# Performance work log

Hardware: AMD Instinct MI355X
Metric: run time of the kernel (lower is better)

The kernel has to match this reference:

```python
import jax, jax.numpy as jnp
import numpy as np

EPS = 1e-5
N_GRID = 519840
N_MESH = 5882
D_DATA = 256
D_NODE = 128
D_EDGE = 2
H = 128


def _ln(x, g, b):
    mu = jnp.mean(x, axis=-1, keepdims=True)
    v = jnp.var(x, axis=-1, keepdims=True)
    return (x - mu) * jax.lax.rsqrt(v + EPS) * g + b


def _ffn(x, Wr, br, W1, b1, W2, b2, g, bn):
    # FFN: norm(residual(x) + Linear(ReLU(Linear(x))))
    res = x if Wr is None else x @ Wr + br
    h = jax.nn.relu(x @ W1 + b1) @ W2 + b2
    return _ln(res + h, g, bn)


def setup_inputs() -> dict:
    key = jax.random.key(0)
    ks = jax.random.split(key, 32)
    s = 0.02

    def w(k, shape):
        return jax.random.normal(k, shape, dtype=jnp.float32) * s

    inp = {}
    inp["x"] = jax.random.normal(ks[0], (N_GRID, D_DATA), dtype=jnp.float32)
    inp["edge_attr"] = jax.random.normal(ks[1], (N_GRID, D_EDGE), dtype=jnp.float32)
    row = jnp.arange(N_GRID, dtype=jnp.int32)
    col = jax.random.randint(ks[2], (N_GRID,), N_GRID, N_GRID + N_MESH, dtype=jnp.int32)
    inp["edge_index"] = jnp.stack([row, col], 0)
    inp["num_mesh"] = N_MESH

    # node_encoder FFN: 256 -> 128 (residual Linear since in != out)
    inp["enc_Wr"] = w(ks[3], (D_DATA, D_NODE)); inp["enc_br"] = jnp.zeros((D_NODE,), jnp.float32)
    inp["enc_W1"] = w(ks[4], (D_DATA, H)); inp["enc_b1"] = jnp.zeros((H,), jnp.float32)
    inp["enc_W2"] = w(ks[5], (H, D_NODE)); inp["enc_b2"] = jnp.zeros((D_NODE,), jnp.float32)
    inp["enc_g"] = jnp.ones((D_NODE,), jnp.float32); inp["enc_bn"] = jnp.zeros((D_NODE,), jnp.float32)

    # edge model FFN: 2*128+2=258 -> 2
    de_in = 2 * D_NODE + D_EDGE
    inp["em_Wr"] = w(ks[6], (de_in, D_EDGE)); inp["em_br"] = jnp.zeros((D_EDGE,), jnp.float32)
    inp["em_W1"] = w(ks[7], (de_in, H)); inp["em_b1"] = jnp.zeros((H,), jnp.float32)
    inp["em_W2"] = w(ks[8], (H, D_EDGE)); inp["em_b2"] = jnp.zeros((D_EDGE,), jnp.float32)
    inp["em_g"] = jnp.ones((D_EDGE,), jnp.float32); inp["em_bn"] = jnp.zeros((D_EDGE,), jnp.float32)

    # node_mlp_1 FFN: 130 -> 130 (identity residual)
    d1 = D_NODE + D_EDGE
    inp["n1_W1"] = w(ks[9], (d1, H)); inp["n1_b1"] = jnp.zeros((H,), jnp.float32)
    inp["n1_W2"] = w(ks[10], (H, d1)); inp["n1_b2"] = jnp.zeros((d1,), jnp.float32)
    inp["n1_g"] = jnp.ones((d1,), jnp.float32); inp["n1_bn"] = jnp.zeros((d1,), jnp.float32)

    # node_mlp_2 FFN: 258 -> 128 (residual Linear)
    d2 = 2 * D_NODE + D_EDGE
    inp["n2_Wr"] = w(ks[11], (d2, D_NODE)); inp["n2_br"] = jnp.zeros((D_NODE,), jnp.float32)
    inp["n2_W1"] = w(ks[12], (d2, H)); inp["n2_b1"] = jnp.zeros((H,), jnp.float32)
    inp["n2_W2"] = w(ks[13], (H, D_NODE)); inp["n2_b2"] = jnp.zeros((D_NODE,), jnp.float32)
    inp["n2_g"] = jnp.ones((D_NODE,), jnp.float32); inp["n2_bn"] = jnp.zeros((D_NODE,), jnp.float32)
    return inp


def reference(x, edge_attr, edge_index, num_mesh,
              enc_Wr, enc_br, enc_W1, enc_b1, enc_W2, enc_b2, enc_g, enc_bn,
              em_Wr, em_br, em_W1, em_b1, em_W2, em_b2, em_g, em_bn,
              n1_W1, n1_b1, n1_W2, n1_b2, n1_g, n1_bn,
              n2_Wr, n2_br, n2_W1, n2_b1, n2_W2, n2_b2, n2_g, n2_bn):
    n_grid = x.shape[0]
    x_hat = _ffn(x, enc_Wr, enc_br, enc_W1, enc_b1, enc_W2, enc_b2, enc_g, enc_bn)
    nodes = jnp.concatenate([x_hat, jnp.zeros((num_mesh, x_hat.shape[1]), x_hat.dtype)], 0)

    row, col = edge_index[0], edge_index[1]
    src = nodes[row]   # [E, 128]
    dest = nodes[col]  # [E, 128]

    # EdgeModel: updated edge_attr
    e = _ffn(jnp.concatenate([src, dest, edge_attr], 1),
             em_Wr, em_br, em_W1, em_b1, em_W2, em_b2, em_g, em_bn) + edge_attr

    # NodeModel: per-edge message, scatter-mean to target nodes
    m = _ffn(jnp.concatenate([src, e], 1),
             None, None, n1_W1, n1_b1, n1_W2, n1_b2, n1_g, n1_bn)  # [E, 130]
    n_tot = n_grid + num_mesh
    s = jax.ops.segment_sum(m, col, num_segments=n_tot)
    cnt = jax.ops.segment_sum(jnp.ones((col.shape[0], 1), m.dtype), col, num_segments=n_tot)
    agg = s / jnp.maximum(cnt, 1.0)  # scatter-mean

    nodes2 = _ffn(jnp.concatenate([nodes, agg], 1),
                  n2_Wr, n2_br, n2_W1, n2_b1, n2_W2, n2_b2, n2_g, n2_bn) + nodes
    return nodes2[n_grid:]
```

## Files before the change

### kernel.cpp

```cpp
#include <hip/hip_runtime.h>
#include <hip/hip_bf16.h>

#define EDGES   519840
#define NGRID   519840
#define NMESH   5882

typedef short s8v __attribute__((ext_vector_type(8)));
typedef float f4v __attribute__((ext_vector_type(4)));

#define OFF_ENC1   0
#define OFF_ENCW2  65536
#define OFF_EM1    81920
#define OFF_N11    104960
#define OFF_N12    125440
#define PACK_EL    143872
#define GSUM_BYTE_OFF  (PACK_EL*2)
#define GSUM_BYTES     (NMESH*130*4)
#define CNT_BYTE_OFF   (GSUM_BYTE_OFF + GSUM_BYTES)
#define CNT_BYTES      (NMESH*4)

__device__ __forceinline__ float b2f(short s) {
  unsigned int u = ((unsigned int)(unsigned short)s) << 16;
  float f; __builtin_memcpy(&f, &u, 4); return f;
}
__device__ __forceinline__ short f2b(float f) {
  __hip_bfloat16 h = __float2bfloat16(f);
  short s; __builtin_memcpy(&s, &h, 2); return s;
}

struct PArgs {
  const float *enc_Wr, *enc_W1, *enc_W2;
  const float *em_Wr, *em_W1, *em_b1, *em_br;
  const float *n1_W1, *n1_b1, *n1_W2;
  short* dst;
};

__global__ __launch_bounds__(256) void kPack(PArgs p) {
  int g = blockIdx.x * 256 + threadIdx.x;
  if (g >= 17984) return;
  short* dst = p.dst;
  if (g < 8192) {
    int s = g >> 10; int rem = g & 1023; int t = rem >> 6; int l = rem & 63;
    int qq = l >> 4, n = (t << 4) + (l & 15);
    s8v v;
    #pragma unroll
    for (int j = 0; j < 8; ++j) {
      int k = s*32 + qq*8 + j;
      v[j] = (n < 128) ? f2b(p.enc_Wr[k*128 + n]) : f2b(p.enc_W1[k*128 + (n-128)]);
    }
    ((s8v*)(dst + OFF_ENC1))[g] = v;
  } else if (g < 10240) {
    int g2 = g - 8192;
    int s = g2 >> 9; int t = (g2 >> 6) & 7; int l = g2 & 63;
    int qq = l >> 4, n = (t << 4) + (l & 15);
    s8v v;
    #pragma unroll
    for (int j = 0; j < 8; ++j) { int k = s*32 + qq*8 + j; v[j] = f2b(p.enc_W2[k*128 + n]); }
    ((s8v*)(dst + OFF_ENCW2))[g2] = v;
  } else if (g < 13120) {
    int g3 = g - 10240;
    int s = g3 / 576; int rem = g3 - s*576; int t = rem >> 6; int l = rem & 63;
    int qq = l >> 4, n = (t << 4) + (l & 15);
    s8v v;
    #pragma unroll
    for (int j = 0; j < 8; ++j) {
      int k = s*32 + qq*8 + j;
      float val = 0.f;
      if (n < 128) {
        if (k < 128)        val = p.em_W1[k*128 + n];
        else if (k < 130)   val = p.em_W1[(128 + k)*128 + n];
        else if (k == 130)  val = p.em_b1[n];
      } else if (n < 130) {
        int h = n - 128;
        if (k < 128)        val = p.em_Wr[k*2 + h];
        else if (k < 130)   val = p.em_Wr[(128 + k)*2 + h];
        else if (k == 130)  val = p.em_br[h];
      }
      v[j] = f2b(val);
    }
    ((s8v*)(dst + OFF_EM1))[g3] = v;
  } else if (g < 15680) {
    int g4 = g - 13120;
    int s = g4 >> 9; int t = (g4 >> 6) & 7; int l = g4 & 63;
    int qq = l >> 4, n = (t << 4) + (l & 15);
    s8v v;
    #pragma unroll
    for (int j = 0; j < 8; ++j) {
      int k = s*32 + qq*8 + j;
      float val = 0.f;
      if (k < 130)       val = p.n1_W1[k*128 + n];
      else if (k == 130) val = p.n1_b1[n];
      v[j] = f2b(val);
    }
    ((s8v*)(dst + OFF_N11))[g4] = v;
  } else {
    int g5 = g - 15680;
    int s = g5 / 576; int rem = g5 - s*576; int t = rem >> 6; int l = rem & 63;
    int qq = l >> 4, n = (t << 4) + (l & 15);
    s8v v;
    #pragma unroll
    for (int j = 0; j < 8; ++j) {
      int k = s*32 + qq*8 + j;
      v[j] = (n < 130) ? f2b(p.n1_W2[k*130 + n]) : (short)0;
    }
    ((s8v*)(dst + OFF_N12))[g5] = v;
  }
}

template<int KS, int MAXT>
__device__ __forceinline__ void run_gemm(const short* A, int strideA,
                                         const short* Bpack, int ntp,
                                         const int* tiles, int nt, int lane,
                                         f4v acc[][MAXT]) {
  const int m = lane & 15, qq = lane >> 4;
  const s8v* Bp = (const s8v*)Bpack;
  #pragma unroll
  for (int s = 0; s < KS; ++s) {
    s8v af[4];
    #pragma unroll
    for (int mt = 0; mt < 4; ++mt)
      af[mt] = *(const s8v*)(A + (mt*16 + m)*strideA + s*32 + qq*8);
    #pragma unroll
    for (int ti = 0; ti < MAXT; ++ti) {
      if (ti < nt) {
        s8v bf = Bp[(s*ntp + tiles[ti])*64 + lane];
        #pragma unroll
        for (int mt = 0; mt < 4; ++mt)
          acc[mt][ti] = __builtin_amdgcn_mfma_f32_16x16x32_bf16(af[mt], bf, acc[mt][ti], 0, 0, 0);
      }
    }
  }
}

struct AArgs {
  const float *x, *eattr;
  const int   *eidx;
  const float *enc_br, *enc_b1, *enc_b2, *enc_g, *enc_bn;
  const float *em_W2, *em_b2, *em_g, *em_bn;
  const float *n1_b2, *n1_g, *n1_bn;
  const short *Penc1, *PencW2, *Pem1, *Pn11, *Pn12;
  float *gsum, *cnt;
};

__global__ __launch_bounds__(256, 2) void kA(AArgs a) {
  __shared__ __align__(16) short ldsP0[64*264];
  __shared__ __align__(16) short ldsH[64*136];
  __shared__ float rowred[64*4*2];
  __shared__ float muv[64*2];
  __shared__ float vbuf[64*2];
  __shared__ float part2[64*4];
  __shared__ int   segv[64];

  const int tid  = threadIdx.x;
  const int lane = tid & 63;
  const int w    = tid >> 6;
  const int m    = lane & 15;
  const int q    = lane >> 4;
  const long row0 = (long)blockIdx.x * 64;

  float ea0 = 0.f, ea1 = 0.f;
  if (tid < 64) {
    long grow = row0 + tid;
    int seg = -1;
    if (grow < EDGES) {
      int cidx = a.eidx[EDGES + grow];
      seg = cidx - NGRID;
      atomicAdd(&a.cnt[seg], 1.0f);
      ea0 = a.eattr[grow*2];
      ea1 = a.eattr[grow*2 + 1];
    }
    segv[tid] = seg;
  }

  for (int i = tid; i < 64*32; i += 256) {
    int r = i >> 5, c = (i & 31) << 3;
    long grow = row0 + r;
    s8v v = {0,0,0,0,0,0,0,0};
    if (grow < EDGES) {
      const float* xr = a.x + grow*256 + c;
      float4 u0 = *(const float4*)(xr);
      float4 u1 = *(const float4*)(xr + 4);
      v[0]=f2b(u0.x); v[1]=f2b(u0.y); v[2]=f2b(u0.z); v[3]=f2b(u0.w);
      v[4]=f2b(u1.x); v[5]=f2b(u1.y); v[6]=f2b(u1.z); v[7]=f2b(u1.w);
    }
    *(s8v*)(ldsP0 + r*264 + c) = v;
  }
  __syncthreads();

  f4v acc1[4][4];
  const f4v fz = {0.f,0.f,0.f,0.f};
  #pragma unroll
  for (int mt = 0; mt < 4; ++mt)
    #pragma unroll
    for (int nt = 0; nt < 4; ++nt) acc1[mt][nt] = fz;
  {
    int tiles[4] = {4*w, 4*w+1, 4*w+2, 4*w+3};
    run_gemm<8,4>(ldsP0, 264, a.Penc1, 16, tiles, 4, lane, acc1);
  }
  __syncthreads();
  float* Rf = (float*)ldsP0;
  if (w < 2) {
    const int cb = w*64;
    #pragma unroll
    for (int nt = 0; nt < 4; ++nt) {
      int col = cb + nt*16 + m;
      float bias = a.enc_br[col];
      #pragma unroll
      for (int mt = 0; mt < 4; ++mt)
        #pragma unroll
        for (int r = 0; r < 4; ++r) {
          int row = mt*16 + q*4 + r;
          Rf[row*132 + col] = acc1[mt][nt][r] + bias;
        }
    }
  } else {
    const int cb = (w-2)*64;
    #pragma unroll
    for (int nt = 0; nt < 4; ++nt) {
      int hc = cb + nt*16 + m;
      float bias = a.enc_b1[hc];
      #pragma unroll
      for (int mt = 0; mt < 4; ++mt)
        #pragma unroll
        for (int r = 0; r < 4; ++r) {
          int row = mt*16 + q*4 + r;
          ldsH[row*136 + hc] = f2b(fmaxf(acc1[mt][nt][r] + bias, 0.f));
        }
    }
  }
  __syncthreads();

  f4v acc2[4][2];
  #pragma unroll
  for (int mt = 0; mt < 4; ++mt) { acc2[mt][0] = fz; acc2[mt][1] = fz; }
  {
    int tiles[2] = {2*w, 2*w+1};
    run_gemm<4,2>(ldsH, 136, a.PencW2, 8, tiles, 2, lane, acc2);
  }
  {
    const int cb = w*32;
    #pragma unroll
    for (int nt = 0; nt < 2; ++nt) {
      int col = cb + nt*16 + m;
      float b2v = a.enc_b2[col];
      #pragma unroll
      for (int mt = 0; mt < 4; ++mt)
        #pragma unroll
        for (int r = 0; r < 4; ++r) {
          int row = mt*16 + q*4 + r;
          acc2[mt][nt][r] += Rf[row*132 + col] + b2v;
        }
    }
  }
  __syncthreads();

  {
    float sA[4][4], qA[4][4];
    #pragma unroll
    for (int mt = 0; mt < 4; ++mt)
      #pragma unroll
      for (int r = 0; r < 4; ++r) {
        float s = 0.f, ss = 0.f;
        #pragma unroll
        for (int nt = 0; nt < 2; ++nt) { float v = acc2[mt][nt][r]; s += v; ss += v*v; }
        sA[mt][r] = s; qA[mt][r] = ss;
      }
    #pragma unroll
    for (int mask = 1; mask <= 8; mask <<= 1)
      #pragma unroll
      for (int mt = 0; mt < 4; ++mt)
        #pragma unroll
        for (int r = 0; r < 4; ++r) {
          sA[mt][r] += __shfl_xor(sA[mt][r], mask);
          qA[mt][r] += __shfl_xor(qA[mt][r], mask);
        }
    if (m == 0) {
      #pragma unroll
      for (int mt = 0; mt < 4; ++mt)
        #pragma unroll
        for (int r = 0; r < 4; ++r) {
          int row = mt*16 + q*4 + r;
          rowred[(row*4 + w)*2]     = sA[mt][r];
          rowred[(row*4 + w)*2 + 1] = qA[mt][r];
        }
    }
  }
  __syncthreads();
  if (tid < 64) {
    float s = 0.f, ss = 0.f;
    #pragma unroll
    for (int ww = 0; ww < 4; ++ww) { s += rowred[(tid*4+ww)*2]; ss += rowred[(tid*4+ww)*2+1]; }
    float mu = s * (1.f/128.f);
    float var = ss * (1.f/128.f) - mu*mu;
    muv[2*tid] = mu; muv[2*tid+1] = rsqrtf(var + 1e-5f);
  }
  __syncthreads();

  short* xh = ldsP0;
  {
    const int cb = w*32;
    #pragma unroll
    for (int nt = 0; nt < 2; ++nt) {
      int col = cb + nt*16 + m;
      float gv = a.enc_g[col], bv = a.enc_bn[col];
      #pragma unroll
      for (int mt = 0; mt < 4; ++mt)
        #pragma unroll
        for (int r = 0; r < 4; ++r) {
          int row = mt*16 + q*4 + r;
          float mu = muv[2*row], rsg = muv[2*row+1];
          xh[row*168 + col] = f2b((acc2[mt][nt][r] - mu)*rsg*gv + bv);
        }
    }
  }
  if (tid < 64) {
    xh[tid*168 + 128] = f2b(ea0);
    xh[tid*168 + 129] = f2b(ea1);
    xh[tid*168 + 130] = (short)0x3f80;
    for (int c = 131; c < 160; ++c) xh[tid*168 + c] = 0;
  }
  __syncthreads();

  int tiles3[3] = {w, w+4, w+8};
  const int nt3 = (w == 0) ? 3 : 2;
  f4v acc3[4][3];
  #pragma unroll
  for (int mt = 0; mt < 4; ++mt) { acc3[mt][0]=fz; acc3[mt][1]=fz; acc3[mt][2]=fz; }
  run_gemm<5,3>(xh, 168, a.Pem1, 9, tiles3, nt3, lane, acc3);
  #pragma unroll
  for (int ti = 0; ti < 3; ++ti) {
    if (ti < nt3) {
      int col = tiles3[ti]*16 + m;
      if (col < 128) {
        #pragma unroll
        for (int mt = 0; mt < 4; ++mt)
          #pragma unroll
          for (int r = 0; r < 4; ++r) {
            int row = mt*16 + q*4 + r;
            ldsH[row*136 + col] = f2b(fmaxf(acc3[mt][ti][r], 0.f));
          }
      } else if (col < 130) {
        #pragma unroll
        for (int mt = 0; mt < 4; ++mt)
          #pragma unroll
          for (int r = 0; r < 4; ++r) {
            int row = mt*16 + q*4 + r;
            vbuf[row*2 + (col - 128)] = acc3[mt][ti][r];
          }
      }
    }
  }
  __syncthreads();

  {
    int r = tid >> 2, p = tid & 3, h = p & 1, kh = p >> 1;
    float s2 = 0.f;
    const short* hb = ldsH + r*136 + kh*64;
    const float* w2 = a.em_W2 + kh*128 + h;
    #pragma unroll 8
    for (int k = 0; k < 64; ++k) s2 += b2f(hb[k]) * w2[2*k];
    part2[tid] = s2;
  }
  __syncthreads();
  if (tid < 128) {
    int r = tid >> 1, h = tid & 1;
    vbuf[r*2+h] = vbuf[r*2+h] + part2[r*4 + h] + part2[r*4 + 2 + h] + a.em_b2[h];
  }
  __syncthreads();
  if (tid < 64) {
    float v0 = vbuf[2*tid], v1 = vbuf[2*tid+1];
    float d = 0.5f*(v0 - v1);
    float rsg = rsqrtf(d*d + 1e-5f);
    float e0 =  d*rsg*a.em_g[0] + a.em_bn[0] + ea0;
    float e1 = -d*rsg*a.em_g[1] + a.em_bn[1] + ea1;
    xh[tid*168 + 128] = f2b(e0);
    xh[tid*168 + 129] = f2b(e1);
  }
  __syncthreads();

  f4v acc4[4][2];
  #pragma unroll
  for (int mt = 0; mt < 4; ++mt) { acc4[mt][0]=fz; acc4[mt][1]=fz; }
  {
    int tiles[2] = {2*w, 2*w+1};
    run_gemm<5,2>(xh, 168, a.Pn11, 8, tiles, 2, lane, acc4);
  }
  {
    const int cb = w*32;
    #pragma unroll
    for (int nt = 0; nt < 2; ++nt) {
      int col = cb + nt*16 + m;
      #pragma unroll
      for (int mt = 0; mt < 4; ++mt)
        #pragma unroll
        for (int r = 0; r < 4; ++r) {
          int row = mt*16 + q*4 + r;
          ldsH[row*136 + col] = f2b(fmaxf(acc4[mt][nt][r], 0.f));
        }
    }
  }
  __syncthreads();

  f4v acc5[4][3];
  #pragma unroll
  for (int mt = 0; mt < 4; ++mt) { acc5[mt][0]=fz; acc5[mt][1]=fz; acc5[mt][2]=fz; }
  run_gemm<4,3>(ldsH, 136, a.Pn12, 9, tiles3, nt3, lane, acc5);

  float gc[3], bnc[3]; int colv[3]; bool cval[3];
  #pragma unroll
  for (int ti = 0; ti < 3; ++ti) {
    cval[ti] = false; colv[ti] = 0; gc[ti] = 0.f; bnc[ti] = 0.f;
    if (ti < nt3) {
      int col = tiles3[ti]*16 + m;
      colv[ti] = col;
      if (col < 130) {
        cval[ti] = true;
        float bias = a.n1_b2[col];
        gc[ti] = a.n1_g[col]; bnc[ti] = a.n1_bn[col];
        #pragma unroll
        for (int mt = 0; mt < 4; ++mt)
          #pragma unroll
          for (int r = 0; r < 4; ++r) {
            int row = mt*16 + q*4 + r;
            acc5[mt][ti][r] += bias + b2f(xh[row*168 + col]);
          }
      }
    }
  }
  {
    float sB[4][4], qB[4][4];
    #pragma unroll
    for (int mt = 0; mt < 4; ++mt)
      #pragma unroll
      for (int r = 0; r < 4; ++r) {
        float s = 0.f, ss = 0.f;
        #pragma unroll
        for (int ti = 0; ti < 3; ++ti)
          if (cval[ti]) { float v = acc5[mt][ti][r]; s += v; ss += v*v; }
        sB[mt][r] = s; qB[mt][r] = ss;
      }
    #pragma unroll
    for (int mask = 1; mask <= 8; mask <<= 1)
      #pragma unroll
      for (int mt = 0; mt < 4; ++mt)
        #pragma unroll
        for (int r = 0; r < 4; ++r) {
          sB[mt][r] += __shfl_xor(sB[mt][r], mask);
          qB[mt][r] += __shfl_xor(qB[mt][r], mask);
        }
    if (m == 0) {
      #pragma unroll
      for (int mt = 0; mt < 4; ++mt)
        #pragma unroll
        for (int r = 0; r < 4; ++r) {
          int row = mt*16 + q*4 + r;
          rowred[(row*4 + w)*2]     = sB[mt][r];
          rowred[(row*4 + w)*2 + 1] = qB[mt][r];
        }
    }
  }
  __syncthreads();
  if (tid < 64) {
    float s = 0.f, ss = 0.f;
    #pragma unroll
    for (int ww = 0; ww < 4; ++ww) { s += rowred[(tid*4+ww)*2]; ss += rowred[(tid*4+ww)*2+1]; }
    float mu = s * (1.f/130.f);
    float var = ss * (1.f/130.f) - mu*mu;
    muv[2*tid] = mu; muv[2*tid+1] = rsqrtf(var + 1e-5f);
  }
  __syncthreads();

  #pragma unroll
  for (int mt = 0; mt < 4; ++mt)
    #pragma unroll
    for (int r = 0; r < 4; ++r) {
      int row = mt*16 + q*4 + r;
      int seg = segv[row];
      if (seg < 0) continue;
      float mu = muv[2*row], rsg = muv[2*row+1];
      #pragma unroll
      for (int ti = 0; ti < 3; ++ti)
        if (cval[ti]) {
          float val = (acc5[mt][ti][r] - mu)*rsg*gc[ti] + bnc[ti];
          atomicAdd(&a.gsum[seg*130 + colv[ti]], val);
        }
    }
}

struct BArgs {
  const float *gsum, *cnt;
  const float *Wr, *br, *W1, *b1, *W2, *b2, *g, *bn;
  float* out;
};

__global__ __launch_bounds__(128) void kB(BArgs b) {
  __shared__ float aggL[130];
  __shared__ float hidL[128];
  __shared__ float red[4];
  int j = threadIdx.x, seg = blockIdx.x;
  float inv = 1.0f / fmaxf(b.cnt[seg], 1.0f);
  for (int c = j; c < 130; c += 128) aggL[c] = b.gsum[seg*130 + c] * inv;
  __syncthreads();
  float resv = b.br[j];
  float hv   = b.b1[j];
  for (int k = 0; k < 130; ++k) {
    float av = aggL[k];
    resv += av * b.Wr[(128 + k)*128 + j];
    hv   += av * b.W1[(128 + k)*128 + j];
  }
  hv = fmaxf(hv, 0.f);
  hidL[j] = hv;
  __syncthreads();
  float ov = b.b2[j];
  for (int k = 0; k < 128; ++k) ov += hidL[k] * b.W2[k*128 + j];
  float sv = resv + ov;
  float s = sv, ss = sv*sv;
  for (int off = 32; off > 0; off >>= 1) { s += __shfl_down(s, off); ss += __shfl_down(ss, off); }
  int wv = j >> 6;
  if ((j & 63) == 0) { red[wv*2] = s; red[wv*2+1] = ss; }
  __syncthreads();
  float S = red[0] + red[2], SS = red[1] + red[3];
  float mu = S * (1.f/128.f);
  float var = SS * (1.f/128.f) - mu*mu;
  float rsg = rsqrtf(var + 1e-5f);
  b.out[seg*128 + j] = (sv - mu)*rsg*b.g[j] + b.bn[j];
}

extern "C" void kernel_launch(void* const* d_in, const int* in_sizes, int n_in,
                              void* d_out, int out_size, void* d_ws, size_t ws_size,
                              hipStream_t stream) {
  const float* x      = (const float*)d_in[0];
  const float* eattr  = (const float*)d_in[1];
  const int*   eidx   = (const int*)d_in[2];
  const float* enc_Wr = (const float*)d_in[4];
  const float* enc_br = (const float*)d_in[5];
  const float* enc_W1 = (const float*)d_in[6];
  const float* enc_b1 = (const float*)d_in[7];
  const float* enc_W2 = (const float*)d_in[8];
  const float* enc_b2 = (const float*)d_in[9];
  const float* enc_g  = (const float*)d_in[10];
  const float* enc_bn = (const float*)d_in[11];
  const float* em_Wr  = (const float*)d_in[12];
  const float* em_br  = (const float*)d_in[13];
  const float* em_W1  = (const float*)d_in[14];
  const float* em_b1  = (const float*)d_in[15];
  const float* em_W2  = (const float*)d_in[16];
  const float* em_b2  = (const float*)d_in[17];
  const float* em_g   = (const float*)d_in[18];
  const float* em_bn  = (const float*)d_in[19];
  const float* n1_W1  = (const float*)d_in[20];
  const float* n1_b1  = (const float*)d_in[21];
  const float* n1_W2  = (const float*)d_in[22];
  const float* n1_b2  = (const float*)d_in[23];
  const float* n1_g   = (const float*)d_in[24];
  const float* n1_bn  = (const float*)d_in[25];
  const float* n2_Wr  = (const float*)d_in[26];
  const float* n2_br  = (const float*)d_in[27];
  const float* n2_W1  = (const float*)d_in[28];
  const float* n2_b1  = (const float*)d_in[29];
  const float* n2_W2  = (const float*)d_in[30];
  const float* n2_b2  = (const float*)d_in[31];
  const float* n2_g   = (const float*)d_in[32];
  const float* n2_bn  = (const float*)d_in[33];

  short* wsP  = (short*)d_ws;
  float* gsum = (float*)((char*)d_ws + GSUM_BYTE_OFF);
  float* cnt  = (float*)((char*)d_ws + CNT_BYTE_OFF);

  hipMemsetAsync(gsum, 0, GSUM_BYTES + CNT_BYTES, stream);

  PArgs pa = { enc_Wr, enc_W1, enc_W2, em_Wr, em_W1, em_b1, em_br, n1_W1, n1_b1, n1_W2, wsP };
  kPack<<<71, 256, 0, stream>>>(pa);

  AArgs aa;
  aa.x = x; aa.eattr = eattr; aa.eidx = eidx;
  aa.enc_br = enc_br; aa.enc_b1 = enc_b1; aa.enc_b2 = enc_b2; aa.enc_g = enc_g; aa.enc_bn = enc_bn;
  aa.em_W2 = em_W2; aa.em_b2 = em_b2; aa.em_g = em_g; aa.em_bn = em_bn;
  aa.n1_b2 = n1_b2; aa.n1_g = n1_g; aa.n1_bn = n1_bn;
  aa.Penc1 = wsP + OFF_ENC1; aa.PencW2 = wsP + OFF_ENCW2;
  aa.Pem1 = wsP + OFF_EM1; aa.Pn11 = wsP + OFF_N11; aa.Pn12 = wsP + OFF_N12;
  aa.gsum = gsum; aa.cnt = cnt;
  kA<<<(EDGES + 63)/64, 256, 0, stream>>>(aa);

  BArgs ba = { gsum, cnt, n2_Wr, n2_br, n2_W1, n2_b1, n2_W2, n2_b2, n2_g, n2_bn, (float*)d_out };
  kB<<<NMESH, 128, 0, stream>>>(ba);
}
```

Measured before the change: 1.515 ms.

## Shrink LDS footprint in kA to raise occupancy to four blocks per CU

The encoder input is now staged in two K-halves through a smaller 64x136 bf16 buffer instead of a full 64x264 buffer. The residual-projection result stays in registers, with tiles reassigned so each wave's residual columns line up with its later output columns, which removes the float LDS round-trip and one barrier. The small scratch arrays are merged or folded into padding slots, and segment ids move to a wave shuffle. Launch bounds ask for 4 blocks per CU, which raises occupancy but adds a barrier in the K loop and tightens the register budget, with a risk of spills.

```diff
diff --git a/kernel.cpp b/kernel.cpp
--- a/kernel.cpp
+++ b/kernel.cpp
@@ -142,14 +142,14 @@
   float *gsum, *cnt;
 };
 
-__global__ __launch_bounds__(256, 2) void kA(AArgs a) {
-  __shared__ __align__(16) short ldsP0[64*264];
+__global__ __launch_bounds__(256, 4) void kA(AArgs a) {
+  __shared__ __align__(16) short ldsX[64*168];
   __shared__ __align__(16) short ldsH[64*136];
-  __shared__ float rowred[64*4*2];
-  __shared__ float muv[64*2];
-  __shared__ float vbuf[64*2];
-  __shared__ float part2[64*4];
-  __shared__ int   segv[64];
+  __shared__ __align__(16) float ldsD[512];
+
+  float* const rowred = ldsD;
+  float* const vbuf   = ldsD;
+  float* const part2  = ldsD + 128;
 
   const int tid  = threadIdx.x;
   const int lane = tid & 63;
@@ -158,34 +158,15 @@
   const int q    = lane >> 4;
   const long row0 = (long)blockIdx.x * 64;
 
+  int segr = -1;
+  if (row0 + lane < EDGES) segr = a.eidx[EDGES + row0 + lane] - NGRID;
+
   float ea0 = 0.f, ea1 = 0.f;
-  if (tid < 64) {
-    long grow = row0 + tid;
-    int seg = -1;
-    if (grow < EDGES) {
-      int cidx = a.eidx[EDGES + grow];
-      seg = cidx - NGRID;
-      atomicAdd(&a.cnt[seg], 1.0f);
-      ea0 = a.eattr[grow*2];
-      ea1 = a.eattr[grow*2 + 1];
-    }
-    segv[tid] = seg;
-  }
-
-  for (int i = tid; i < 64*32; i += 256) {
-    int r = i >> 5, c = (i & 31) << 3;
-    long grow = row0 + r;
-    s8v v = {0,0,0,0,0,0,0,0};
-    if (grow < EDGES) {
-      const float* xr = a.x + grow*256 + c;
-      float4 u0 = *(const float4*)(xr);
-      float4 u1 = *(const float4*)(xr + 4);
-      v[0]=f2b(u0.x); v[1]=f2b(u0.y); v[2]=f2b(u0.z); v[3]=f2b(u0.w);
-      v[4]=f2b(u1.x); v[5]=f2b(u1.y); v[6]=f2b(u1.z); v[7]=f2b(u1.w);
-    }
-    *(s8v*)(ldsP0 + r*264 + c) = v;
-  }
-  __syncthreads();
+  if (tid < 64 && segr >= 0) {
+    atomicAdd(&a.cnt[segr], 1.0f);
+    ea0 = a.eattr[(row0 + tid)*2];
+    ea1 = a.eattr[(row0 + tid)*2 + 1];
+  }
 
   f4v acc1[4][4];
   const f4v fz = {0.f,0.f,0.f,0.f};
@@ -193,40 +174,37 @@
   for (int mt = 0; mt < 4; ++mt)
     #pragma unroll
     for (int nt = 0; nt < 4; ++nt) acc1[mt][nt] = fz;
-  {
-    int tiles[4] = {4*w, 4*w+1, 4*w+2, 4*w+3};
-    run_gemm<8,4>(ldsP0, 264, a.Penc1, 16, tiles, 4, lane, acc1);
-  }
-  __syncthreads();
-  float* Rf = (float*)ldsP0;
-  if (w < 2) {
-    const int cb = w*64;
-    #pragma unroll
-    for (int nt = 0; nt < 4; ++nt) {
-      int col = cb + nt*16 + m;
-      float bias = a.enc_br[col];
-      #pragma unroll
-      for (int mt = 0; mt < 4; ++mt)
-        #pragma unroll
-        for (int r = 0; r < 4; ++r) {
-          int row = mt*16 + q*4 + r;
-          Rf[row*132 + col] = acc1[mt][nt][r] + bias;
-        }
-    }
-  } else {
-    const int cb = (w-2)*64;
-    #pragma unroll
-    for (int nt = 0; nt < 4; ++nt) {
-      int hc = cb + nt*16 + m;
-      float bias = a.enc_b1[hc];
-      #pragma unroll
-      for (int mt = 0; mt < 4; ++mt)
-        #pragma unroll
-        for (int r = 0; r < 4; ++r) {
-          int row = mt*16 + q*4 + r;
-          ldsH[row*136 + hc] = f2b(fmaxf(acc1[mt][nt][r] + bias, 0.f));
-        }
-    }
+
+  const int tiles1[4] = {2*w, 2*w+1, 8+2*w, 9+2*w};
+
+  #pragma unroll
+  for (int half = 0; half < 2; ++half) {
+    if (half) __syncthreads();
+    for (int i = tid; i < 64*16; i += 256) {
+      int r = i >> 4, c = (i & 15) << 3;
+      s8v v = {0,0,0,0,0,0,0,0};
+      if (row0 + r < EDGES) {
+        const float* xr = a.x + (row0 + r)*256 + half*128 + c;
+        float4 u0 = *(const float4*)(xr);
+        float4 u1 = *(const float4*)(xr + 4);
+        v[0]=f2b(u0.x); v[1]=f2b(u0.y); v[2]=f2b(u0.z); v[3]=f2b(u0.w);
+        v[4]=f2b(u1.x); v[5]=f2b(u1.y); v[6]=f2b(u1.z); v[7]=f2b(u1.w);
+      }
+      *(s8v*)(ldsX + r*136 + c) = v;
+    }
+    __syncthreads();
+    run_gemm<4,4>(ldsX, 136, a.Penc1 + half*(4*16*64*8), 16, tiles1, 4, lane, acc1);
+  }
+
+  #pragma unroll
+  for (int ti = 2; ti < 4; ++ti) {
+    int hc = (tiles1[ti] - 8)*16 + m;
+    float bias = a.enc_b1[hc];
+    #pragma unroll
+    for (int mt = 0; mt < 4; ++mt)
+      #pragma unroll
+      for (int r = 0; r < 4; ++r)
+        ldsH[(mt*16 + q*4 + r)*136 + hc] = f2b(fmaxf(acc1[mt][ti][r] + bias, 0.f));
   }
   __syncthreads();
 
@@ -237,22 +215,16 @@
     int tiles[2] = {2*w, 2*w+1};
     run_gemm<4,2>(ldsH, 136, a.PencW2, 8, tiles, 2, lane, acc2);
   }
-  {
-    const int cb = w*32;
-    #pragma unroll
-    for (int nt = 0; nt < 2; ++nt) {
-      int col = cb + nt*16 + m;
-      float b2v = a.enc_b2[col];
-      #pragma unroll
-      for (int mt = 0; mt < 4; ++mt)
-        #pragma unroll
-        for (int r = 0; r < 4; ++r) {
-          int row = mt*16 + q*4 + r;
-          acc2[mt][nt][r] += Rf[row*132 + col] + b2v;
-        }
-    }
-  }
-  __syncthreads();
+  #pragma unroll
+  for (int nt = 0; nt < 2; ++nt) {
+    int col = (2*w + nt)*16 + m;
+    float bb = a.enc_br[col] + a.enc_b2[col];
+    #pragma unroll
+    for (int mt = 0; mt < 4; ++mt)
+      #pragma unroll
+      for (int r = 0; r < 4; ++r)
+        acc2[mt][nt][r] += acc1[mt][nt][r] + bb;
+  }
 
   {
     float sA[4][4], qA[4][4];
@@ -292,31 +264,30 @@
     for (int ww = 0; ww < 4; ++ww) { s += rowred[(tid*4+ww)*2]; ss += rowred[(tid*4+ww)*2+1]; }
     float mu = s * (1.f/128.f);
     float var = ss * (1.f/128.f) - mu*mu;
-    muv[2*tid] = mu; muv[2*tid+1] = rsqrtf(var + 1e-5f);
-  }
-  __syncthreads();
-
-  short* xh = ldsP0;
-  {
-    const int cb = w*32;
-    #pragma unroll
-    for (int nt = 0; nt < 2; ++nt) {
-      int col = cb + nt*16 + m;
-      float gv = a.enc_g[col], bv = a.enc_bn[col];
-      #pragma unroll
-      for (int mt = 0; mt < 4; ++mt)
-        #pragma unroll
-        for (int r = 0; r < 4; ++r) {
-          int row = mt*16 + q*4 + r;
-          float mu = muv[2*row], rsg = muv[2*row+1];
-          xh[row*168 + col] = f2b((acc2[mt][nt][r] - mu)*rsg*gv + bv);
-        }
-    }
+    float* mv = (float*)(ldsX + tid*168 + 160);
+    mv[0] = mu; mv[1] = rsqrtf(var + 1e-5f);
+  }
+  __syncthreads();
+
+  short* const xh = ldsX;
+  #pragma unroll
+  for (int nt = 0; nt < 2; ++nt) {
+    int col = (2*w + nt)*16 + m;
+    float gv = a.enc_g[col], bv = a.enc_bn[col];
+    #pragma unroll
+    for (int mt = 0; mt < 4; ++mt)
+      #pragma unroll
+      for (int r = 0; r < 4; ++r) {
+        int row = mt*16 + q*4 + r;
+        const float* mv = (const float*)(ldsX + row*168 + 160);
+        xh[row*168 + col] = f2b((acc2[mt][nt][r] - mv[0])*mv[1]*gv + bv);
+      }
   }
   if (tid < 64) {
     xh[tid*168 + 128] = f2b(ea0);
     xh[tid*168 + 129] = f2b(ea1);
     xh[tid*168 + 130] = (short)0x3f80;
+    #pragma unroll
     for (int c = 131; c < 160; ++c) xh[tid*168 + c] = 0;
   }
   __syncthreads();
@@ -364,7 +335,7 @@
   __syncthreads();
   if (tid < 128) {
     int r = tid >> 1, h = tid & 1;
-    vbuf[r*2+h] = vbuf[r*2+h] + part2[r*4 + h] + part2[r*4 + 2 + h] + a.em_b2[h];
+    vbuf[tid] = vbuf[tid] + part2[r*4 + h] + part2[r*4 + 2 + h] + a.em_b2[h];
   }
   __syncthreads();
   if (tid < 64) {
@@ -385,19 +356,16 @@
     int tiles[2] = {2*w, 2*w+1};
     run_gemm<5,2>(xh, 168, a.Pn11, 8, tiles, 2, lane, acc4);
   }
-  {
-    const int cb = w*32;
-    #pragma unroll
-    for (int nt = 0; nt < 2; ++nt) {
-      int col = cb + nt*16 + m;
-      #pragma unroll
-      for (int mt = 0; mt < 4; ++mt)
-        #pragma unroll
-        for (int r = 0; r < 4; ++r) {
-          int row = mt*16 + q*4 + r;
-          ldsH[row*136 + col] = f2b(fmaxf(acc4[mt][nt][r], 0.f));
-        }
-    }
+  #pragma unroll
+  for (int nt = 0; nt < 2; ++nt) {
+    int col = (2*w + nt)*16 + m;
+    #pragma unroll
+    for (int mt = 0; mt < 4; ++mt)
+      #pragma unroll
+      for (int r = 0; r < 4; ++r) {
+        int row = mt*16 + q*4 + r;
+        ldsH[row*136 + col] = f2b(fmaxf(acc4[mt][nt][r], 0.f));
+      }
   }
   __syncthreads();
 
@@ -466,7 +434,8 @@
     for (int ww = 0; ww < 4; ++ww) { s += rowred[(tid*4+ww)*2]; ss += rowred[(tid*4+ww)*2+1]; }
     float mu = s * (1.f/130.f);
     float var = ss * (1.f/130.f) - mu*mu;
-    muv[2*tid] = mu; muv[2*tid+1] = rsqrtf(var + 1e-5f);
+    float* mv = (float*)(ldsX + tid*168 + 160);
+    mv[0] = mu; mv[1] = rsqrtf(var + 1e-5f);
   }
   __syncthreads();
 
@@ -475,9 +444,10 @@
     #pragma unroll
     for (int r = 0; r < 4; ++r) {
       int row = mt*16 + q*4 + r;
-      int seg = segv[row];
+      int seg = __shfl(segr, row);
       if (seg < 0) continue;
-      float mu = muv[2*row], rsg = muv[2*row+1];
+      const float* mv = (const float*)(ldsX + row*168 + 160);
+      float mu = mv[0], rsg = mv[1];
       #pragma unroll
       for (int ti = 0; ti < 3; ++ti)
         if (cval[ti]) {
```

Result: faster. 1.426 ms (-5.9%).
